# Performance work log

Hardware: AMD Instinct MI355X
Metric: run time of the kernel (lower is better)

Reference implementation:

```python
import jax, jax.numpy as jnp
import numpy as np

N = 100000          # num nodes
E_C = 6_400_000     # connection edges
E_D = 400_000       # destination edges
F_IN = 5
H = 8
BN_EPS = 1e-5
L2_EPS = 1e-12


def setup_inputs() -> dict:
    key = jax.random.key(0)
    ks = jax.random.split(key, 16)
    d = {}
    d["x"] = jax.random.normal(ks[0], (N, F_IN), dtype=jnp.float32)
    d["edge_index_connections"] = jax.random.randint(ks[1], (2, E_C), 0, N, dtype=jnp.int64)
    d["edge_index_destinations"] = jax.random.randint(ks[2], (2, E_D), 0, N, dtype=jnp.int64)
    # SAGEConv weights: lin_l (neighbor aggregate), lin_r (root), no bias
    d["W1l"] = jax.random.normal(ks[3], (H, F_IN), jnp.float32) * 0.3
    d["W1r"] = jax.random.normal(ks[4], (H, F_IN), jnp.float32) * 0.3
    d["W2l"] = jax.random.normal(ks[5], (H, H), jnp.float32) * 0.3
    d["W2r"] = jax.random.normal(ks[6], (H, H), jnp.float32) * 0.3
    d["W3l"] = jax.random.normal(ks[7], (H, H), jnp.float32) * 0.3
    d["W3r"] = jax.random.normal(ks[8], (H, H), jnp.float32) * 0.3
    d["W4l"] = jax.random.normal(ks[9], (H, H), jnp.float32) * 0.3
    d["W4r"] = jax.random.normal(ks[10], (H, H), jnp.float32) * 0.3
    # LazyBatchNorm1d affine params (init gamma=1, beta=0)
    for i in range(1, 5):
        d[f"g{i}"] = jnp.ones((H,), jnp.float32)
        d[f"b{i}"] = jnp.zeros((H,), jnp.float32)
    return d


def _sage(x, ei, Wl, Wr):
    # PyG SAGEConv(mean aggr, normalize=True, bias=False):
    # out = lin_l(mean_{j in N(i)} x_j) + lin_r(x_i); then L2 normalize rows.
    src, dst = ei[0], ei[1]
    msgs = x[src]                                            # [E, F] gather
    s = jax.ops.segment_sum(msgs, dst, num_segments=N)       # [N, F]
    cnt = jax.ops.segment_sum(jnp.ones((ei.shape[1],), x.dtype), dst, num_segments=N)
    mean = s / jnp.maximum(cnt, 1.0)[:, None]                # zero for isolated nodes
    out = mean @ Wl.T + x @ Wr.T                             # [N, H]
    nrm = jnp.linalg.norm(out, axis=-1, keepdims=True)
    return out / jnp.maximum(nrm, L2_EPS)


def _bn(x, g, b):
    # BatchNorm1d in training mode: per-feature batch stats (biased variance)
    m = x.mean(axis=0)
    v = x.var(axis=0)
    return (x - m) * jax.lax.rsqrt(v + BN_EPS) * g + b


def reference(x, edge_index_connections, edge_index_destinations,
              W1l, W1r, W2l, W2r, W3l, W3r, W4l, W4r,
              g1, b1, g2, b2, g3, b3, g4, b4):
    eic = edge_index_connections
    eid = edge_index_destinations
    h = _bn(jax.nn.relu(_sage(x, eic, W1l, W1r)), g1, b1)
    # ITERATIONS_BEFORE_DESTINATION = 1 (conv4 + bn2)
    h = _bn(jax.nn.relu(_sage(h, eic, W4l, W4r)), g2, b2)
    # destination pass (conv2 + bn3)
    h = _bn(jax.nn.relu(_sage(h, eid, W2l, W2r)), g3, b3)
    # ITERATIONS_AFTER_DESTINATION = 2 (conv3 + bn4)
    for _ in range(2):
        h = _bn(jax.nn.relu(_sage(h, eic, W3l, W3r)), g4, b4)
    return h
```

## Files before the change

kernel.cpp:

```cpp
#include <hip/hip_runtime.h>
#include <hip/hip_fp16.h>

#define NN 100000
#define EC 6400000
#define ED 400000
#define BN_EPS 1e-5f
#define NB 391
#define CAPC 18432
#define CAPD 2048
#define EPB 8192
#define NBK_C 782
#define NBK_D 49
#define PREPB 16


__global__ __launch_bounds__(1024)
void zero_small(int* __restrict__ cnt_c, int* __restrict__ cnt_d,
                float* __restrict__ stats) {
    int t = threadIdx.x;
    for (int i = t; i < NB; i += 1024) { cnt_c[i] = 0; cnt_d[i] = 0; }
    for (int i = t; i < 5 * 256; i += 1024) stats[i] = 0.f;
}

__global__ __launch_bounds__(1024)
void scatter_fused(const int* __restrict__ eic, const int* __restrict__ eid,
                   int* __restrict__ cnt_c, int* __restrict__ cnt_d,
                   unsigned* __restrict__ packed_c, unsigned* __restrict__ packed_d,
                   const float* __restrict__ x, const float* __restrict__ W1l,
                   const float* __restrict__ W1r, float* __restrict__ xp,
                   __half* __restrict__ xp16,
                   float* __restrict__ W1lp, float* __restrict__ W1rp) {
    int blk = blockIdx.x;
    int tid = threadIdx.x;
    if (blk >= NBK_C + NBK_D) {
        int pb = blk - (NBK_C + NBK_D);
        int t = pb * 1024 + tid;
        if (t < 64) {
            int f = t >> 3, k = t & 7;
            W1lp[t] = (k < 5) ? W1l[f * 5 + k] : 0.f;
            W1rp[t] = (k < 5) ? W1r[f * 5 + k] : 0.f;
        }
        for (int idx = t; idx < NN * 8; idx += PREPB * 1024) {
            int f = idx & 7, i = idx >> 3;
            float v = (f < 5) ? x[i * 5 + f] : 0.f;
            xp[idx] = v;
            xp16[idx] = __float2half(v);
        }
        return;
    }
    const int* ei; int E, cap, base; int* cnt; unsigned* packed;
    if (blk < NBK_C) { ei = eic; E = EC; cnt = cnt_c; packed = packed_c; cap = CAPC; base = blk; }
    else             { ei = eid; E = ED; cnt = cnt_d; packed = packed_d; cap = CAPD; base = blk - NBK_C; }

    __shared__ int h[NB];
    __shared__ int lbase[NB];
    __shared__ int lcur[NB];
    __shared__ int dg[NB];
    __shared__ int ws[16];
    __shared__ int sbuf[EPB];
    __shared__ unsigned short sbkt[EPB];

    for (int i = tid; i < NB; i += 1024) h[i] = 0;
    __syncthreads();
    int beg = base * EPB, end = min(E, beg + EPB);
    int ecnt = end - beg;
    for (int e = beg + tid * 4; e < end; e += 4096) {
        int4 d4 = *(const int4*)&ei[E + e];
        atomicAdd(&h[d4.x >> 8], 1);
        atomicAdd(&h[d4.y >> 8], 1);
        atomicAdd(&h[d4.z >> 8], 1);
        atomicAdd(&h[d4.w >> 8], 1);
    }
    __syncthreads();
    {
        int v = (tid < NB) ? h[tid] : 0;
        int lane = tid & 63, w = tid >> 6;
        int xx = v;
        #pragma unroll
        for (int sh = 1; sh < 64; sh <<= 1) { int y = __shfl_up(xx, sh); if (lane >= sh) xx += y; }
        if (lane == 63) ws[w] = xx;
        __syncthreads();
        int wb = 0;
        #pragma unroll
        for (int j = 0; j < 16; ++j) if (j < w) wb += ws[j];
        int excl = wb + xx - v;
        if (tid < NB) {
            lbase[tid] = excl;
            lcur[tid] = excl;
            int gb = v ? atomicAdd(&cnt[tid], v) : 0;
            dg[tid] = gb - excl;
        }
    }
    __syncthreads();
    for (int e = beg + tid * 4; e < end; e += 4096) {
        int4 s4 = *(const int4*)&ei[e];
        int4 d4 = *(const int4*)&ei[E + e];
        { int b = d4.x >> 8; int p = atomicAdd(&lcur[b], 1); sbuf[p] = s4.x | ((d4.x & 255) << 17); sbkt[p] = (unsigned short)b; }
        { int b = d4.y >> 8; int p = atomicAdd(&lcur[b], 1); sbuf[p] = s4.y | ((d4.y & 255) << 17); sbkt[p] = (unsigned short)b; }
        { int b = d4.z >> 8; int p = atomicAdd(&lcur[b], 1); sbuf[p] = s4.z | ((d4.z & 255) << 17); sbkt[p] = (unsigned short)b; }
        { int b = d4.w >> 8; int p = atomicAdd(&lcur[b], 1); sbuf[p] = s4.w | ((d4.w & 255) << 17); sbkt[p] = (unsigned short)b; }
    }
    __syncthreads();
    for (int j = tid; j < ecnt; j += 1024) {
        int b = sbkt[j];
        unsigned idx = (unsigned)(dg[b] + j);
        if (idx < (unsigned)cap)
            packed[(size_t)b * cap + idx] = (unsigned)sbuf[j];
    }
}

__global__ __launch_bounds__(1024)
void csr_sort(const unsigned* __restrict__ packed_c, const int* __restrict__ cnt_c,
              int* __restrict__ csr_c, int* __restrict__ offs_c,
              int* __restrict__ deg_c, float* __restrict__ inv_c,
              const unsigned* __restrict__ packed_d, const int* __restrict__ cnt_d,
              int* __restrict__ csr_d, int* __restrict__ offs_d,
              int* __restrict__ deg_d, float* __restrict__ inv_d) {
    __shared__ int h[256];
    __shared__ int loff[256];
    __shared__ int ws[4];
    __shared__ int ebuf[CAPC];
    int blk = blockIdx.x;
    const unsigned* packed; const int* cnt; int cap, b;
    int* csr; int* offs; int* deg; float* inv;
    if (blk < NB) { packed = packed_c; cnt = cnt_c; cap = CAPC; b = blk;
                    csr = csr_c; offs = offs_c; deg = deg_c; inv = inv_c; }
    else          { packed = packed_d; cnt = cnt_d; cap = CAPD; b = blk - NB;
                    csr = csr_d; offs = offs_d; deg = deg_d; inv = inv_d; }
    int tid = threadIdx.x;
    size_t ebeg = (size_t)b * cap;
    int ecnt = min(cnt[b], cap);
    int node0 = b << 8;
    int nn = min(256, NN - node0);
    if (tid < 256) h[tid] = 0;
    __syncthreads();
    for (int e = tid; e < ecnt; e += 1024)
        atomicAdd(&h[packed[ebeg + e] >> 17], 1);
    __syncthreads();
    int v = (tid < 256) ? h[tid] : 0;
    {
        int lane = tid & 63, w = tid >> 6;
        int xx = v;
        #pragma unroll
        for (int sh = 1; sh < 64; sh <<= 1) { int y = __shfl_up(xx, sh); if (lane >= sh) xx += y; }
        if (lane == 63 && w < 4) ws[w] = xx;
        __syncthreads();
        if (tid < 256) {
            int wb = 0;
            #pragma unroll
            for (int j = 0; j < 4; ++j) if (j < w) wb += ws[j];
            int excl = wb + xx - v;
            loff[tid] = excl;
            if (tid < nn) {
                int node = node0 + tid;
                offs[node] = (int)ebeg + excl;
                deg[node]  = v;
                inv[node]  = 1.0f / (float)(v > 1 ? v : 1);
            }
        }
    }
    __syncthreads();
    for (int e = tid; e < ecnt; e += 1024) {
        unsigned u = packed[ebeg + e];
        int p = atomicAdd(&loff[u >> 17], 1);
        ebuf[p] = (int)(u & 0x1FFFF);
    }
    __syncthreads();
    for (int e = tid; e < ecnt; e += 1024) csr[ebeg + e] = ebuf[e];
}

#define ACC8(RV, M) do { \
    float2 q0 = __half22float2(*(const __half2*)&RV.x); \
    float2 q1 = __half22float2(*(const __half2*)&RV.y); \
    float2 q2 = __half22float2(*(const __half2*)&RV.z); \
    float2 q3 = __half22float2(*(const __half2*)&RV.w); \
    a0 = fmaf(q0.x, M, a0); a1 = fmaf(q0.y, M, a1); \
    a2 = fmaf(q1.x, M, a2); a3 = fmaf(q1.y, M, a3); \
    a4 = fmaf(q2.x, M, a4); a5 = fmaf(q2.y, M, a5); \
    a6 = fmaf(q3.x, M, a6); a7 = fmaf(q3.y, M, a7); \
} while (0)

template<bool APPLY_BN>
__global__ __launch_bounds__(256)
void sage_layer8(const float* __restrict__ hin,
                 const __half* __restrict__ hin16,
                 const float* __restrict__ stats_in,
                 const float* __restrict__ gin, const float* __restrict__ bin,
                 const int* __restrict__ offs, const int* __restrict__ deg,
                 const int* __restrict__ csr, const float* __restrict__ inv,
                 const float* __restrict__ Wl, const float* __restrict__ Wr,
                 float* __restrict__ hout, __half* __restrict__ hout16,
                 float* __restrict__ stats_out) {
    __shared__ float bl[16];
    int tid = threadIdx.x;
    if (tid < 16) bl[tid] = 0.f;
    __syncthreads();
    int wave = tid >> 6, lane = tid & 63, g = lane >> 3, f = lane & 7;

    float wls[8], wrs[8];
    float Bl = 0.f, Br = 0.f;
    #pragma unroll
    for (int k = 0; k < 8; ++k) {
        float w_l = Wl[f * 8 + k], w_r = Wr[f * 8 + k];
        float sck = 1.f, shk = 0.f;
        if constexpr (APPLY_BN) {
            float m = stats_in[k * 16] * (1.f / NN);
            float v = stats_in[(8 + k) * 16] * (1.f / NN) - m * m;
            float is = rsqrtf(v + BN_EPS);
            sck = gin[k] * is;
            shk = bin[k] - m * sck;
        }
        wls[k] = sck * w_l;
        wrs[k] = sck * w_r;
        Bl = fmaf(shk, w_l, Bl);
        Br = fmaf(shk, w_r, Br);
    }

    float acc_r = 0.f, acc_r2 = 0.f;
    const int stride = gridDim.x * 32;
    for (int i0 = (blockIdx.x * 4 + wave) * 8; i0 < NN; i0 += stride) {
        int i = i0 + g;
        int ic = min(i, NN - 1);
        bool ok = (i < NN);
        int d = ok ? deg[ic] : 0;
        int o = offs[ic];
        float im = inv[ic];
        const float4* hp = (const float4*)(hin + (size_t)ic * 8);
        float4 h0 = hp[0];
        float4 h1 = hp[1];
        float a0 = 0, a1 = 0, a2 = 0, a3 = 0, a4 = 0, a5 = 0, a6 = 0, a7 = 0;
        for (int b = 0; b < d; b += 32) {
            int e = b + f * 4;
            const int* cp = csr + o + e;
            int c0 = cp[0], c1 = cp[1], c2 = cp[2], c3 = cp[3];
            bool k0 = (e < d), k1 = (e + 1 < d), k2 = (e + 2 < d), k3 = (e + 3 < d);
            unsigned s0 = k0 ? ((unsigned)c0 & 0x1FFFFu) : 0u;
            unsigned s1 = k1 ? ((unsigned)c1 & 0x1FFFFu) : 0u;
            unsigned s2 = k2 ? ((unsigned)c2 & 0x1FFFFu) : 0u;
            unsigned s3 = k3 ? ((unsigned)c3 & 0x1FFFFu) : 0u;
            uint4 r0 = *(const uint4*)(hin16 + (size_t)s0 * 8);
            uint4 r1 = *(const uint4*)(hin16 + (size_t)s1 * 8);
            uint4 r2 = *(const uint4*)(hin16 + (size_t)s2 * 8);
            uint4 r3 = *(const uint4*)(hin16 + (size_t)s3 * 8);
            float m0 = k0 ? 1.f : 0.f;
            float m1 = k1 ? 1.f : 0.f;
            float m2 = k2 ? 1.f : 0.f;
            float m3 = k3 ? 1.f : 0.f;
            ACC8(r0, m0);
            ACC8(r1, m1);
            ACC8(r2, m2);
            ACC8(r3, m3);
        }
        #pragma unroll
        for (int msk = 1; msk < 8; msk <<= 1) {
            a0 += __shfl_xor(a0, msk); a1 += __shfl_xor(a1, msk);
            a2 += __shfl_xor(a2, msk); a3 += __shfl_xor(a3, msk);
            a4 += __shfl_xor(a4, msk); a5 += __shfl_xor(a5, msk);
            a6 += __shfl_xor(a6, msk); a7 += __shfl_xor(a7, msk);
        }
        float dnz = (d > 0) ? 1.f : 0.f;
        float hk[8] = { h0.x, h0.y, h0.z, h0.w, h1.x, h1.y, h1.z, h1.w };
        float ac[8] = { a0, a1, a2, a3, a4, a5, a6, a7 };
        float y = fmaf(dnz, Bl, Br);
        #pragma unroll
        for (int k = 0; k < 8; ++k) {
            y = fmaf(ac[k] * im, wls[k], y);
            y = fmaf(hk[k], wrs[k], y);
        }
        float n2 = y * y;
        n2 += __shfl_xor(n2, 1);
        n2 += __shfl_xor(n2, 2);
        n2 += __shfl_xor(n2, 4);
        float z = y / fmaxf(sqrtf(n2), 1e-12f);
        float r = fmaxf(z, 0.f);
        r = ok ? r : 0.f;
        if (ok) {
            hout[(size_t)i * 8 + f] = r;
            hout16[(size_t)i * 8 + f] = __float2half(r);
        }
        acc_r += r;
        acc_r2 += r * r;
    }
    atomicAdd(&bl[f], acc_r);
    atomicAdd(&bl[8 + f], acc_r2);
    __syncthreads();
    if (tid < 16) atomicAdd(&stats_out[tid * 16], bl[tid]);
}

__global__ void apply_bn_out(const float* __restrict__ hin,
                             const float* __restrict__ stats,
                             const float* __restrict__ g, const float* __restrict__ b,
                             float* __restrict__ out) {
    int t = blockIdx.x * blockDim.x + threadIdx.x;
    if (t >= NN * 8) return;
    int f = t & 7;
    float m = stats[f * 16] * (1.0f / NN);
    float v = stats[(8 + f) * 16] * (1.0f / NN) - m * m;
    float sc = g[f] * rsqrtf(v + BN_EPS);
    float sh = b[f] - m * sc;
    out[t] = fmaf(hin[t], sc, sh);
}


static inline char* bump(char*& p, size_t bytes) {
    char* r = p;
    p += (bytes + 255) & ~(size_t)255;
    return r;
}

extern "C" void kernel_launch(void* const* d_in, const int* in_sizes, int n_in,
                              void* d_out, int out_size, void* d_ws, size_t ws_size,
                              hipStream_t stream) {
    const float* x   = (const float*)d_in[0];
    const int* eic   = (const int*)d_in[1];
    const int* eid   = (const int*)d_in[2];
    const float* W1l = (const float*)d_in[3];
    const float* W1r = (const float*)d_in[4];
    const float* W2l = (const float*)d_in[5];
    const float* W2r = (const float*)d_in[6];
    const float* W3l = (const float*)d_in[7];
    const float* W3r = (const float*)d_in[8];
    const float* W4l = (const float*)d_in[9];
    const float* W4r = (const float*)d_in[10];
    const float* g1 = (const float*)d_in[11];
    const float* b1 = (const float*)d_in[12];
    const float* g2 = (const float*)d_in[13];
    const float* b2 = (const float*)d_in[14];
    const float* g3 = (const float*)d_in[15];
    const float* b3 = (const float*)d_in[16];
    const float* g4 = (const float*)d_in[17];
    const float* b4 = (const float*)d_in[18];
    float* out = (float*)d_out;

    char* p = (char*)d_ws;
    float* stats   = (float*)bump(p, 5 * 256 * 4);
    int*   cnt_c   = (int*)  bump(p, NB * 4);
    int*   cnt_d   = (int*)  bump(p, NB * 4);
    int*   offs_c  = (int*)  bump(p, NN * 4);
    int*   deg_c   = (int*)  bump(p, NN * 4);
    float* inv_c   = (float*)bump(p, NN * 4);
    int*   offs_d  = (int*)  bump(p, NN * 4);
    int*   deg_d   = (int*)  bump(p, NN * 4);
    float* inv_d   = (float*)bump(p, NN * 4);
    int*   csr_c   = (int*)  bump(p, ((size_t)NB * CAPC + 256) * 4);
    int*   csr_d   = (int*)  bump(p, ((size_t)NB * CAPD + 256) * 4);
    float* xp32    = (float*)bump(p, (size_t)NN * 8 * 4);
    __half* xp16   = (__half*)bump(p, (size_t)NN * 8 * 2);
    float* W1lp    = (float*)bump(p, 64 * 4);
    float* W1rp    = (float*)bump(p, 64 * 4);
    unsigned* packed_d = (unsigned*)bump(p, (size_t)NB * CAPD * 4);
    char* pc = p;
    unsigned* packed_c = (unsigned*)bump(p, (size_t)NB * CAPC * 4);
    char* pr = pc;
    float*  r_a   = (float*) bump(pr, (size_t)NN * 8 * 4);
    float*  r_b   = (float*) bump(pr, (size_t)NN * 8 * 4);
    __half* h16_a = (__half*)bump(pr, (size_t)NN * 8 * 2);
    __half* h16_b = (__half*)bump(pr, (size_t)NN * 8 * 2);
    (void)ws_size; (void)in_sizes; (void)n_in; (void)out_size;

    zero_small<<<1, 1024, 0, stream>>>(cnt_c, cnt_d, stats);
    scatter_fused<<<NBK_C + NBK_D + PREPB, 1024, 0, stream>>>(
        eic, eid, cnt_c, cnt_d, packed_c, packed_d,
        x, W1l, W1r, xp32, xp16, W1lp, W1rp);
    csr_sort<<<2 * NB, 1024, 0, stream>>>(
        packed_c, cnt_c, csr_c, offs_c, deg_c, inv_c,
        packed_d, cnt_d, csr_d, offs_d, deg_d, inv_d);

    const int LB = 2048;
    sage_layer8<false><<<LB, 256, 0, stream>>>(
        xp32, xp16, nullptr, nullptr, nullptr,
        offs_c, deg_c, csr_c, inv_c, W1lp, W1rp, r_a, h16_a, stats + 0);
    sage_layer8<true><<<LB, 256, 0, stream>>>(
        r_a, h16_a, stats + 0, g1, b1,
        offs_c, deg_c, csr_c, inv_c, W4l, W4r, r_b, h16_b, stats + 256);
    sage_layer8<true><<<LB, 256, 0, stream>>>(
        r_b, h16_b, stats + 256, g2, b2,
        offs_d, deg_d, csr_d, inv_d, W2l, W2r, r_a, h16_a, stats + 512);
    sage_layer8<true><<<LB, 256, 0, stream>>>(
        r_a, h16_a, stats + 512, g3, b3,
        offs_c, deg_c, csr_c, inv_c, W3l, W3r, r_b, h16_b, stats + 768);
    sage_layer8<true><<<LB, 256, 0, stream>>>(
        r_b, h16_b, stats + 768, g4, b4,
        offs_c, deg_c, csr_c, inv_c, W3l, W3r, r_a, h16_a, stats + 1024);
    apply_bn_out<<<(NN * 8 + 255) / 256, 256, 0, stream>>>(r_a, stats + 1024, g4, b4, out);
}
```

Baseline: 526.8 us.

## Sort connection CSR by source tile and aggregate from LDS-staged feature tiles

The connection-graph CSR is re-sorted within each destination by source tile (16 tiles of 6250 nodes), and per-node per-tile counts are stored. A new tiled SAGE kernel stages each fp16 feature tile (100 KB) into shared memory and gathers neighbours from LDS instead of random global/L2 reads. One thread handles each node, with 196 blocks of 512 threads. The aim is to cut random gather traffic, at the cost of low occupancy from the large LDS footprint, 16 sequential tile loads per block, serial per-thread edge loops with degree imbalance, and extra sorting work.

```diff
diff --git a/kernel.cpp b/kernel.cpp
--- a/kernel.cpp
+++ b/kernel.cpp
@@ -12,6 +12,7 @@
 #define NBK_C 782
 #define NBK_D 49
 #define PREPB 16
+#define TIL 6250
 
 
 __global__ __launch_bounds__(1024)
@@ -53,7 +54,6 @@
     else             { ei = eid; E = ED; cnt = cnt_d; packed = packed_d; cap = CAPD; base = blk - NBK_C; }
 
     __shared__ int h[NB];
-    __shared__ int lbase[NB];
     __shared__ int lcur[NB];
     __shared__ int dg[NB];
     __shared__ int ws[16];
@@ -85,7 +85,6 @@
         for (int j = 0; j < 16; ++j) if (j < w) wb += ws[j];
         int excl = wb + xx - v;
         if (tid < NB) {
-            lbase[tid] = excl;
             lcur[tid] = excl;
             int gb = v ? atomicAdd(&cnt[tid], v) : 0;
             dg[tid] = gb - excl;
@@ -111,62 +110,245 @@
 
 __global__ __launch_bounds__(1024)
 void csr_sort(const unsigned* __restrict__ packed_c, const int* __restrict__ cnt_c,
-              int* __restrict__ csr_c, int* __restrict__ offs_c,
-              int* __restrict__ deg_c, float* __restrict__ inv_c,
+              int* __restrict__ csr_c, int* __restrict__ offs_c, float* __restrict__ inv_c,
+              unsigned short* __restrict__ cnt16,
               const unsigned* __restrict__ packed_d, const int* __restrict__ cnt_d,
               int* __restrict__ csr_d, int* __restrict__ offs_d,
               int* __restrict__ deg_d, float* __restrict__ inv_d) {
-    __shared__ int h[256];
-    __shared__ int loff[256];
-    __shared__ int ws[4];
+    __shared__ int h4[4096];
+    __shared__ int ws[16];
     __shared__ int ebuf[CAPC];
-    int blk = blockIdx.x;
-    const unsigned* packed; const int* cnt; int cap, b;
-    int* csr; int* offs; int* deg; float* inv;
-    if (blk < NB) { packed = packed_c; cnt = cnt_c; cap = CAPC; b = blk;
-                    csr = csr_c; offs = offs_c; deg = deg_c; inv = inv_c; }
-    else          { packed = packed_d; cnt = cnt_d; cap = CAPD; b = blk - NB;
-                    csr = csr_d; offs = offs_d; deg = deg_d; inv = inv_d; }
-    int tid = threadIdx.x;
-    size_t ebeg = (size_t)b * cap;
-    int ecnt = min(cnt[b], cap);
-    int node0 = b << 8;
-    int nn = min(256, NN - node0);
-    if (tid < 256) h[tid] = 0;
-    __syncthreads();
-    for (int e = tid; e < ecnt; e += 1024)
-        atomicAdd(&h[packed[ebeg + e] >> 17], 1);
-    __syncthreads();
-    int v = (tid < 256) ? h[tid] : 0;
-    {
-        int lane = tid & 63, w = tid >> 6;
-        int xx = v;
-        #pragma unroll
-        for (int sh = 1; sh < 64; sh <<= 1) { int y = __shfl_up(xx, sh); if (lane >= sh) xx += y; }
-        if (lane == 63 && w < 4) ws[w] = xx;
-        __syncthreads();
-        if (tid < 256) {
+    int blk = blockIdx.x, tid = threadIdx.x;
+    if (blk < NB) {
+        int b = blk;
+        size_t ebeg = (size_t)b * CAPC;
+        int ecnt = min(cnt_c[b], CAPC);
+        int node0 = b << 8;
+        for (int i = tid; i < 4096; i += 1024) h4[i] = 0;
+        __syncthreads();
+        for (int e = tid; e < ecnt; e += 1024) {
+            unsigned u = packed_c[ebeg + e];
+            int dl = (int)(u >> 17);
+            int src = (int)(u & 0x1FFFFu);
+            atomicAdd(&h4[(dl << 4) | (src / TIL)], 1);
+        }
+        __syncthreads();
+        int i0 = tid * 4;
+        int v0 = h4[i0], v1 = h4[i0 + 1], v2 = h4[i0 + 2], v3 = h4[i0 + 3];
+        int s = v0 + v1 + v2 + v3;
+        {
+            int lane = tid & 63, w = tid >> 6;
+            int xx = s;
+            #pragma unroll
+            for (int sh = 1; sh < 64; sh <<= 1) { int y = __shfl_up(xx, sh); if (lane >= sh) xx += y; }
+            if (lane == 63) ws[w] = xx;
+            __syncthreads();
             int wb = 0;
             #pragma unroll
-            for (int j = 0; j < 4; ++j) if (j < w) wb += ws[j];
-            int excl = wb + xx - v;
-            loff[tid] = excl;
-            if (tid < nn) {
-                int node = node0 + tid;
-                offs[node] = (int)ebeg + excl;
-                deg[node]  = v;
-                inv[node]  = 1.0f / (float)(v > 1 ? v : 1);
+            for (int j = 0; j < 16; ++j) if (j < w) wb += ws[j];
+            int e0 = wb + xx - s;
+            h4[i0] = e0;
+            h4[i0 + 1] = e0 + v0;
+            h4[i0 + 2] = e0 + v0 + v1;
+            h4[i0 + 3] = e0 + v0 + v1 + v2;
+        }
+        __syncthreads();
+        for (int i = tid; i < 4096; i += 1024) {
+            int node = node0 + (i >> 4);
+            if (node < NN) {
+                int st = h4[i];
+                int en = (i == 4095) ? ecnt : h4[i + 1];
+                cnt16[(size_t)node * 16 + (i & 15)] = (unsigned short)(en - st);
             }
         }
-    }
-    __syncthreads();
-    for (int e = tid; e < ecnt; e += 1024) {
-        unsigned u = packed[ebeg + e];
-        int p = atomicAdd(&loff[u >> 17], 1);
-        ebuf[p] = (int)(u & 0x1FFFF);
-    }
-    __syncthreads();
-    for (int e = tid; e < ecnt; e += 1024) csr[ebeg + e] = ebuf[e];
+        if (tid < 256) {
+            int node = node0 + tid;
+            if (node < NN) {
+                int st = h4[tid << 4];
+                int en = (tid == 255) ? ecnt : h4[(tid + 1) << 4];
+                int dgc = en - st;
+                offs_c[node] = (int)ebeg + st;
+                inv_c[node] = 1.0f / (float)(dgc > 1 ? dgc : 1);
+            }
+        }
+        __syncthreads();
+        for (int e = tid; e < ecnt; e += 1024) {
+            unsigned u = packed_c[ebeg + e];
+            int dl = (int)(u >> 17);
+            int src = (int)(u & 0x1FFFFu);
+            int p = atomicAdd(&h4[(dl << 4) | (src / TIL)], 1);
+            ebuf[p] = src;
+        }
+        __syncthreads();
+        for (int e = tid; e < ecnt; e += 1024) csr_c[ebeg + e] = ebuf[e];
+    } else {
+        int b = blk - NB;
+        int* h = h4;
+        int* loff = h4 + 256;
+        size_t ebeg = (size_t)b * CAPD;
+        int ecnt = min(cnt_d[b], CAPD);
+        int node0 = b << 8;
+        int nn = min(256, NN - node0);
+        if (tid < 256) h[tid] = 0;
+        __syncthreads();
+        for (int e = tid; e < ecnt; e += 1024)
+            atomicAdd(&h[packed_d[ebeg + e] >> 17], 1);
+        __syncthreads();
+        int v = (tid < 256) ? h[tid] : 0;
+        {
+            int lane = tid & 63, w = tid >> 6;
+            int xx = v;
+            #pragma unroll
+            for (int sh = 1; sh < 64; sh <<= 1) { int y = __shfl_up(xx, sh); if (lane >= sh) xx += y; }
+            if (lane == 63 && w < 4) ws[w] = xx;
+            __syncthreads();
+            if (tid < 256) {
+                int wb = 0;
+                #pragma unroll
+                for (int j = 0; j < 4; ++j) if (j < w) wb += ws[j];
+                int excl = wb + xx - v;
+                loff[tid] = excl;
+                if (tid < nn) {
+                    int node = node0 + tid;
+                    offs_d[node] = (int)ebeg + excl;
+                    deg_d[node] = v;
+                    inv_d[node] = 1.0f / (float)(v > 1 ? v : 1);
+                }
+            }
+        }
+        __syncthreads();
+        for (int e = tid; e < ecnt; e += 1024) {
+            unsigned u = packed_d[ebeg + e];
+            int p = atomicAdd(&loff[u >> 17], 1);
+            ebuf[p] = (int)(u & 0x1FFFFu);
+        }
+        __syncthreads();
+        for (int e = tid; e < ecnt; e += 1024) csr_d[ebeg + e] = ebuf[e];
+    }
+}
+
+template<bool APPLY_BN>
+__global__ __launch_bounds__(512)
+void sage_tiled(const float* __restrict__ hin, const __half* __restrict__ hin16,
+                const float* __restrict__ stats_in,
+                const float* __restrict__ gin, const float* __restrict__ bin,
+                const int* __restrict__ offs, const unsigned short* __restrict__ cnt16,
+                const int* __restrict__ csr, const float* __restrict__ inv,
+                const float* __restrict__ Wl, const float* __restrict__ Wr,
+                float* __restrict__ hout, __half* __restrict__ hout16,
+                float* __restrict__ stats_out) {
+    __shared__ uint4 tile[TIL];
+    __shared__ float wl[64], wr[64];
+    __shared__ float bl[16];
+    int tid = threadIdx.x;
+    if (tid < 64) { wl[tid] = Wl[tid]; wr[tid] = Wr[tid]; }
+    if (tid < 16) bl[tid] = 0.f;
+    int n = blockIdx.x * 512 + tid;
+    bool ok = (n < NN);
+    int nc = ok ? n : NN - 1;
+    int cur = offs[nc];
+    float im = inv[nc];
+    const uint4* c16 = (const uint4*)(cnt16 + (size_t)nc * 16);
+    uint4 ca = c16[0], cb = c16[1];
+    unsigned cw[8] = { ca.x, ca.y, ca.z, ca.w, cb.x, cb.y, cb.z, cb.w };
+
+    float a0 = 0, a1 = 0, a2 = 0, a3 = 0, a4 = 0, a5 = 0, a6 = 0, a7 = 0;
+    int dsum = 0;
+    #pragma unroll
+    for (int t = 0; t < 16; ++t) {
+        __syncthreads();
+        const uint4* sp = (const uint4*)hin16 + t * TIL;
+        for (int r = tid; r < TIL; r += 512) tile[r] = sp[r];
+        __syncthreads();
+        unsigned wv = cw[t >> 1];
+        int c = (t & 1) ? (int)(wv >> 16) : (int)(wv & 0xFFFFu);
+        if (!ok) c = 0;
+        dsum += c;
+        int base = t * TIL;
+        for (int k = 0; k < c; ++k) {
+            int u = csr[cur++];
+            uint4 rv = tile[u - base];
+            float2 p0 = __half22float2(*(const __half2*)&rv.x);
+            float2 p1 = __half22float2(*(const __half2*)&rv.y);
+            float2 p2 = __half22float2(*(const __half2*)&rv.z);
+            float2 p3 = __half22float2(*(const __half2*)&rv.w);
+            a0 += p0.x; a1 += p0.y; a2 += p1.x; a3 += p1.y;
+            a4 += p2.x; a5 += p2.y; a6 += p3.x; a7 += p3.y;
+        }
+    }
+
+    float ac[8] = { a0, a1, a2, a3, a4, a5, a6, a7 };
+    float dnz = (dsum > 0) ? 1.f : 0.f;
+    const float4* hp = (const float4*)(hin + (size_t)nc * 8);
+    float4 h0 = hp[0], h1 = hp[1];
+    float hk[8] = { h0.x, h0.y, h0.z, h0.w, h1.x, h1.y, h1.z, h1.w };
+    float ag[8], hh[8];
+    #pragma unroll
+    for (int k = 0; k < 8; ++k) {
+        float sck = 1.f, shk = 0.f;
+        if constexpr (APPLY_BN) {
+            float m = stats_in[k * 16] * (1.f / NN);
+            float v = stats_in[(8 + k) * 16] * (1.f / NN) - m * m;
+            float is = rsqrtf(v + BN_EPS);
+            sck = gin[k] * is;
+            shk = bin[k] - m * sck;
+        }
+        ag[k] = fmaf(sck, ac[k] * im, shk * dnz);
+        hh[k] = fmaf(sck, hk[k], shk);
+    }
+    float y[8];
+    #pragma unroll
+    for (int f = 0; f < 8; ++f) y[f] = 0.f;
+    #pragma unroll
+    for (int k = 0; k < 8; ++k) {
+        #pragma unroll
+        for (int f = 0; f < 8; ++f) {
+            y[f] = fmaf(ag[k], wl[f * 8 + k], y[f]);
+            y[f] = fmaf(hh[k], wr[f * 8 + k], y[f]);
+        }
+    }
+    float n2 = 0.f;
+    #pragma unroll
+    for (int f = 0; f < 8; ++f) n2 += y[f] * y[f];
+    float rn = 1.0f / fmaxf(sqrtf(n2), 1e-12f);
+    float r[8];
+    #pragma unroll
+    for (int f = 0; f < 8; ++f) {
+        float z = fmaxf(y[f] * rn, 0.f);
+        r[f] = ok ? z : 0.f;
+    }
+    if (ok) {
+        float4 o0 = { r[0], r[1], r[2], r[3] };
+        float4 o1 = { r[4], r[5], r[6], r[7] };
+        ((float4*)(hout + (size_t)n * 8))[0] = o0;
+        ((float4*)(hout + (size_t)n * 8))[1] = o1;
+        __half2 q0 = __floats2half2_rn(r[0], r[1]);
+        __half2 q1 = __floats2half2_rn(r[2], r[3]);
+        __half2 q2 = __floats2half2_rn(r[4], r[5]);
+        __half2 q3 = __floats2half2_rn(r[6], r[7]);
+        uint4 ov = { *(unsigned*)&q0, *(unsigned*)&q1, *(unsigned*)&q2, *(unsigned*)&q3 };
+        *(uint4*)(hout16 + (size_t)n * 8) = ov;
+    }
+    float r2[8];
+    #pragma unroll
+    for (int f = 0; f < 8; ++f) r2[f] = r[f] * r[f];
+    #pragma unroll
+    for (int m = 1; m < 64; m <<= 1) {
+        #pragma unroll
+        for (int f = 0; f < 8; ++f) {
+            r[f] += __shfl_xor(r[f], m);
+            r2[f] += __shfl_xor(r2[f], m);
+        }
+    }
+    if ((tid & 63) == 0) {
+        #pragma unroll
+        for (int f = 0; f < 8; ++f) {
+            atomicAdd(&bl[f], r[f]);
+            atomicAdd(&bl[8 + f], r2[f]);
+        }
+    }
+    __syncthreads();
+    if (tid < 16) atomicAdd(&stats_out[tid * 16], bl[tid]);
 }
 
 #define ACC8(RV, M) do { \
@@ -260,11 +442,11 @@
         }
         float dnz = (d > 0) ? 1.f : 0.f;
         float hk[8] = { h0.x, h0.y, h0.z, h0.w, h1.x, h1.y, h1.z, h1.w };
-        float ac[8] = { a0, a1, a2, a3, a4, a5, a6, a7 };
+        float acv[8] = { a0, a1, a2, a3, a4, a5, a6, a7 };
         float y = fmaf(dnz, Bl, Br);
         #pragma unroll
         for (int k = 0; k < 8; ++k) {
-            y = fmaf(ac[k] * im, wls[k], y);
+            y = fmaf(acv[k] * im, wls[k], y);
             y = fmaf(hk[k], wrs[k], y);
         }
         float n2 = y * y;
@@ -337,11 +519,11 @@
     int*   cnt_c   = (int*)  bump(p, NB * 4);
     int*   cnt_d   = (int*)  bump(p, NB * 4);
     int*   offs_c  = (int*)  bump(p, NN * 4);
-    int*   deg_c   = (int*)  bump(p, NN * 4);
     float* inv_c   = (float*)bump(p, NN * 4);
     int*   offs_d  = (int*)  bump(p, NN * 4);
     int*   deg_d   = (int*)  bump(p, NN * 4);
     float* inv_d   = (float*)bump(p, NN * 4);
+    unsigned short* cnt16 = (unsigned short*)bump(p, (size_t)NN * 16 * 2);
     int*   csr_c   = (int*)  bump(p, ((size_t)NB * CAPC + 256) * 4);
     int*   csr_d   = (int*)  bump(p, ((size_t)NB * CAPD + 256) * 4);
     float* xp32    = (float*)bump(p, (size_t)NN * 8 * 4);
@@ -363,24 +545,24 @@
         eic, eid, cnt_c, cnt_d, packed_c, packed_d,
         x, W1l, W1r, xp32, xp16, W1lp, W1rp);
     csr_sort<<<2 * NB, 1024, 0, stream>>>(
-        packed_c, cnt_c, csr_c, offs_c, deg_c, inv_c,
+        packed_c, cnt_c, csr_c, offs_c, inv_c, cnt16,
         packed_d, cnt_d, csr_d, offs_d, deg_d, inv_d);
 
-    const int LB = 2048;
-    sage_layer8<false><<<LB, 256, 0, stream>>>(
+    const int TB = 196;
+    sage_tiled<false><<<TB, 512, 0, stream>>>(
         xp32, xp16, nullptr, nullptr, nullptr,
-        offs_c, deg_c, csr_c, inv_c, W1lp, W1rp, r_a, h16_a, stats + 0);
-    sage_layer8<true><<<LB, 256, 0, stream>>>(
+        offs_c, cnt16, csr_c, inv_c, W1lp, W1rp, r_a, h16_a, stats + 0);
+    sage_tiled<true><<<TB, 512, 0, stream>>>(
         r_a, h16_a, stats + 0, g1, b1,
-        offs_c, deg_c, csr_c, inv_c, W4l, W4r, r_b, h16_b, stats + 256);
-    sage_layer8<true><<<LB, 256, 0, stream>>>(
+        offs_c, cnt16, csr_c, inv_c, W4l, W4r, r_b, h16_b, stats + 256);
+    sage_layer8<true><<<2048, 256, 0, stream>>>(
         r_b, h16_b, stats + 256, g2, b2,
         offs_d, deg_d, csr_d, inv_d, W2l, W2r, r_a, h16_a, stats + 512);
-    sage_layer8<true><<<LB, 256, 0, stream>>>(
+    sage_tiled<true><<<TB, 512, 0, stream>>>(
         r_a, h16_a, stats + 512, g3, b3,
-        offs_c, deg_c, csr_c, inv_c, W3l, W3r, r_b, h16_b, stats + 768);
-    sage_layer8<true><<<LB, 256, 0, stream>>>(
+        offs_c, cnt16, csr_c, inv_c, W3l, W3r, r_b, h16_b, stats + 768);
+    sage_tiled<true><<<TB, 512, 0, stream>>>(
         r_b, h16_b, stats + 768, g4, b4,
-        offs_c, deg_c, csr_c, inv_c, W3l, W3r, r_a, h16_a, stats + 1024);
+        offs_c, cnt16, csr_c, inv_c, W3l, W3r, r_a, h16_a, stats + 1024);
     apply_bn_out<<<(NN * 8 + 255) / 256, 256, 0, stream>>>(r_a, stats + 1024, g4, b4, out);
 }
```

Result: slower. 632.4 us (+20.1%).
